# Optimization experiments

Measured on AMD Instinct MI355X. Metric: run time of the kernel, lower is better.

## Reference

```python
import jax, jax.numpy as jnp
import numpy as np

B, H, W, ENC = 64, 14, 14, 2048
A, E, D, V, T = 512, 512, 512, 10000, 21


def setup_inputs() -> dict:
    key = jax.random.key(0)
    ks = jax.random.split(key, 24)
    f = lambda k, shape, s: (jax.random.normal(k, shape, jnp.float32) * s)
    inp = {
        'encoder_out': f(ks[0], (B, H, W, ENC), 1.0),
        'encoded_captions': jax.random.randint(ks[1], (B, T), 0, V),
        'caption_lengths': jax.random.randint(ks[2], (B,), 0, T + 1),
        'emb': jax.random.uniform(ks[3], (V, E), jnp.float32, -0.1, 0.1),
        'enc_att_W': f(ks[4], (ENC, A), 0.02), 'enc_att_b': jnp.zeros((A,), jnp.float32),
        'dec_att_W': f(ks[5], (D, A), 0.04), 'dec_att_b': jnp.zeros((A,), jnp.float32),
        'full_att_W': f(ks[6], (A, 1), 0.04), 'full_att_b': jnp.zeros((1,), jnp.float32),
        'init_h_W': f(ks[7], (ENC, D), 0.02), 'init_h_b': jnp.zeros((D,), jnp.float32),
        'init_c_W': f(ks[8], (ENC, D), 0.02), 'init_c_b': jnp.zeros((D,), jnp.float32),
        'f_beta_W': f(ks[9], (D, ENC), 0.04), 'f_beta_b': jnp.zeros((ENC,), jnp.float32),
        'W_ih': f(ks[10], (4 * D, E + ENC), 0.02), 'b_ih': jnp.zeros((4 * D,), jnp.float32),
        'W_hh': f(ks[11], (4 * D, D), 0.04), 'b_hh': jnp.zeros((4 * D,), jnp.float32),
        'fc_W': jax.random.uniform(ks[12], (D, V), jnp.float32, -0.1, 0.1),
        'fc_b': jnp.zeros((V,), jnp.float32),
    }
    return inp


def reference(encoder_out, encoded_captions, caption_lengths, emb,
              enc_att_W, enc_att_b, dec_att_W, dec_att_b, full_att_W, full_att_b,
              init_h_W, init_h_b, init_c_W, init_c_b, f_beta_W, f_beta_b,
              W_ih, b_ih, W_hh, b_hh, fc_W, fc_b):
    b = encoder_out.shape[0]
    enc = encoder_out.reshape(b, -1, encoder_out.shape[-1])  # (B, P, ENC)
    cl = jnp.clip(caption_lengths.reshape(-1), 1, None)
    sort_ind = jnp.argsort(-cl)  # descending by length
    cl = cl[sort_ind]
    enc = enc[sort_ind]
    caps = encoded_captions[sort_ind]
    dec_len = cl - 1  # (B,)

    embs = emb[caps]  # (B, T, E)
    mean_enc = enc.mean(axis=1)
    h0 = jnp.tanh(mean_enc @ init_h_W + init_h_b)
    c0 = jnp.tanh(mean_enc @ init_c_W + init_c_b)

    att1 = enc @ enc_att_W + enc_att_b  # (B, P, A), loop-invariant
    Tdec = caps.shape[1] - 1
    embs_t = jnp.swapaxes(embs[:, :Tdec], 0, 1)  # (Tdec, B, E)

    def step(carry, xs):
        h, c = carry
        t, x_emb = xs
        active = (t < dec_len)[:, None]  # (B,1)
        att2 = h @ dec_att_W + dec_att_b  # (B, A)
        e = jnp.squeeze(jax.nn.relu(att1 + att2[:, None, :]) @ full_att_W, -1) + full_att_b[0]  # (B,P)
        alpha = jax.nn.softmax(e + 1e-8, axis=1)
        awe = jnp.einsum('bpe,bp->be', enc, alpha)  # (B, ENC)
        gate = jax.nn.sigmoid(h @ f_beta_W + f_beta_b)
        awe = gate * awe
        x = jnp.concatenate([x_emb, awe], axis=1)  # (B, E+ENC)
        gates = x @ W_ih.T + b_ih + h @ W_hh.T + b_hh  # (B, 4D)
        i, f, g, o = jnp.split(gates, 4, axis=1)
        c_new = jax.nn.sigmoid(f) * c + jax.nn.sigmoid(i) * jnp.tanh(g)
        h_new = jax.nn.sigmoid(o) * jnp.tanh(c_new)
        preds = h_new @ fc_W + fc_b
        h = jnp.where(active, h_new, h)
        c = jnp.where(active, c_new, c)
        preds = jnp.where(active, preds, 0.0)
        alpha = jnp.where(active, alpha, 0.0)
        return (h, c), (preds, alpha)

    (_, _), (preds, alphas) = jax.lax.scan(step, (h0, c0), (jnp.arange(Tdec), embs_t))
    predictions = jnp.swapaxes(preds, 0, 1)  # (B, Tdec, V)
    alphas = jnp.swapaxes(alphas, 0, 1)      # (B, Tdec, P)
    return predictions, caps, dec_len, alphas, sort_ind
```

## Files before the change

### kernel.cpp

```cpp
#include <hip/hip_runtime.h>
#include <cstddef>


namespace {

typedef _Float16 f16;
typedef f16 f16x8 __attribute__((ext_vector_type(8)));
typedef f16 f16x4 __attribute__((ext_vector_type(4)));
typedef f16 f16x2 __attribute__((ext_vector_type(2)));
typedef float f32x4 __attribute__((ext_vector_type(4)));

constexpr int NB = 64, NP = 196, NE = 2048, NA = 512, ND = 512, NV = 10000;
constexpr int NT_CAP = 21, NTD = 20;
constexpr int KC = 3072;
constexpr int LDT = 40;
constexpr int LDK = 72;

constexpr size_t OFF_ATT1   = 0;
constexpr size_t OFF_DAW    = 12845056;
constexpr size_t OFF_FBW    = 13369344;
constexpr size_t OFF_EAW    = 15466496;
constexpr size_t OFF_IHW    = 17563648;
constexpr size_t OFF_ICW    = 19660800;
constexpr size_t OFF_FCW    = 15466496;
constexpr size_t OFF_WCAT   = 25755648;
constexpr size_t OFF_MEAN16 = 38338560;
constexpr size_t OFF_H16    = 38600704;
constexpr size_t OFF_HNEW16 = 38666240;
constexpr size_t OFF_C      = 38731776;
constexpr size_t OFF_ATT2   = 38862848;
constexpr size_t OFF_GATE   = 38993920;
constexpr size_t OFF_ALPHA  = 39518208;
constexpr size_t OFF_XCAT   = 39569408;
constexpr size_t OFF_INT    = 39962624;
constexpr size_t OFF_BCAT   = 39970816;
constexpr size_t OFF_ENC16  = 39979008;
constexpr size_t FULL_BYTES = 91359232;
constexpr size_t OFF_HSEQ   = FULL_BYTES;
constexpr size_t FULL2_BYTES = FULL_BYTES + (size_t)NTD * NB * ND * 2;

__device__ __forceinline__ float sigmoidf_(float x) { return 1.0f / (1.0f + expf(-x)); }

__device__ __forceinline__ void stage16(const f16* __restrict__ src, int lda, int k0,
                                        f16* __restrict__ lds, int tid) {
  const int row = tid >> 2, seg = tid & 3;
  *(f16x8*)&lds[row * LDT + seg * 8] =
      *(const f16x8*)&src[(size_t)row * lda + k0 + seg * 8];
}

__device__ __forceinline__ void cvt8(const float* __restrict__ p, f16* __restrict__ dst) {
  const float4 a = *(const float4*)p;
  const float4 b = *(const float4*)(p + 4);
  f16x8 v;
  v[0] = (f16)a.x; v[1] = (f16)a.y; v[2] = (f16)a.z; v[3] = (f16)a.w;
  v[4] = (f16)b.x; v[5] = (f16)b.y; v[6] = (f16)b.z; v[7] = (f16)b.w;
  *(f16x8*)dst = v;
}

__device__ __forceinline__ void wave_gemm64(const f16* __restrict__ A,
                                            const f16* __restrict__ Brow, int K,
                                            int kbeg, int kend,
                                            int col, int quad, f32x4* acc) {
  for (int k0 = kbeg; k0 < kend; k0 += 32) {
    const int kk = k0 + quad * 8;
    const f16x8 b = *(const f16x8*)&Brow[(size_t)col * K + kk];
#pragma unroll
    for (int mt = 0; mt < 4; ++mt) {
      const f16x8 a = *(const f16x8*)&A[(size_t)(mt * 16 + col) * K + kk];
      acc[mt] = __builtin_amdgcn_mfma_f32_16x16x32_f16(a, b, acc[mt], 0, 0, 0);
    }
  }
}

__global__ void k_sort(const int* __restrict__ cap_len, const int* __restrict__ caps,
                       int* __restrict__ perm, int* __restrict__ declen,
                       int* __restrict__ caps_sorted,
                       float* __restrict__ out_caps, float* __restrict__ out_declen,
                       float* __restrict__ out_sortind) {
  __shared__ int cl[NB];
  __shared__ int pr[NB];
  const int i = threadIdx.x;
  int c = cap_len[i];
  if (c < 1) c = 1;
  cl[i] = c;
  __syncthreads();
  int rank = 0;
  for (int j = 0; j < NB; ++j) {
    const int cj = cl[j];
    if (cj > c || (cj == c && j < i)) rank++;
  }
  pr[rank] = i;
  __syncthreads();
  const int src = pr[i];
  perm[i] = src;
  const int dl = cl[src] - 1;
  declen[i] = dl;
  out_declen[i] = (float)dl;
  out_sortind[i] = (float)src;
  for (int j = 0; j < NT_CAP; ++j) {
    const int v = caps[src * NT_CAP + j];
    caps_sorted[i * NT_CAP + j] = v;
    out_caps[i * NT_CAP + j] = (float)v;
  }
}

__global__ __launch_bounds__(256) void k_tconv(const float* __restrict__ src,
                                               f16* __restrict__ dst, int K, int Nsrc) {
  __shared__ float tile[32][33];
  const int n0 = blockIdx.x * 32, k0 = blockIdx.y * 32;
  const int tid = threadIdx.x;
  const int a = tid & 31, q = tid >> 5;
#pragma unroll
  for (int r = 0; r < 4; ++r) {
    const int kl = q * 4 + r;
    tile[a][kl] = (n0 + a < Nsrc) ? src[(size_t)(k0 + kl) * Nsrc + n0 + a] : 0.0f;
  }
  __syncthreads();
#pragma unroll
  for (int r = 0; r < 4; ++r) {
    const int nl = q * 4 + r;
    dst[(size_t)(n0 + nl) * K + k0 + a] = (f16)tile[nl][a];
  }
}

__global__ __launch_bounds__(256) void k_cvt_wcat2(const float* __restrict__ Wih,
                                                   const float* __restrict__ Whh,
                                                   const float* __restrict__ bih,
                                                   const float* __restrict__ bhh,
                                                   f16* __restrict__ Wcat2,
                                                   float* __restrict__ bcat) {
  const int r = blockIdx.x;
  const int d = r >> 2, g = r & 3;
  const int n = g * 512 + d;
  for (int k = threadIdx.x; k < KC; k += 256) {
    const float v = (k < 2560) ? Wih[(size_t)n * 2560 + k] : Whh[(size_t)n * 512 + (k - 2560)];
    Wcat2[(size_t)r * KC + k] = (f16)v;
  }
  if (threadIdx.x == 0) bcat[r] = bih[n] + bhh[n];
}

__global__ __launch_bounds__(256) void k_mean(const float* __restrict__ enc,
                                              const int* __restrict__ perm,
                                              f16* __restrict__ mean16) {
  const int b = blockIdx.y;
  const int c0 = blockIdx.x * 512 + threadIdx.x * 2;
  const float* base = enc + (size_t)perm[b] * NP * NE + c0;
  float a0 = 0.0f, a1 = 0.0f;
  for (int p = 0; p < NP; ++p) {
    const float2 v = *(const float2*)&base[(size_t)p * NE];
    a0 += v.x; a1 += v.y;
  }
  mean16[(size_t)b * NE + c0] = (f16)(a0 * (1.0f / (float)NP));
  mean16[(size_t)b * NE + c0 + 1] = (f16)(a1 * (1.0f / (float)NP));
}

__global__ __launch_bounds__(256) void k_mean16(const f16* __restrict__ enc16,
                                                f16* __restrict__ mean16) {
  const int b = blockIdx.y;
  const int c0 = blockIdx.x * 512 + threadIdx.x * 2;
  const f16* base = enc16 + (size_t)b * NP * NE + c0;
  float a0 = 0.0f, a1 = 0.0f;
  for (int p = 0; p < NP; ++p) {
    const f16x2 v = *(const f16x2*)&base[(size_t)p * NE];
    a0 += (float)v[0]; a1 += (float)v[1];
  }
  mean16[(size_t)b * NE + c0] = (f16)(a0 * (1.0f / (float)NP));
  mean16[(size_t)b * NE + c0 + 1] = (f16)(a1 * (1.0f / (float)NP));
}

__global__ __launch_bounds__(256) void k_enc_cvt(const float* __restrict__ enc,
                                                 const int* __restrict__ perm,
                                                 f16* __restrict__ enc16) {
  const int p = blockIdx.x, b = blockIdx.y;
  const float* src = enc + ((size_t)perm[b] * NP + p) * NE;
  f16* dst = enc16 + ((size_t)b * NP + p) * NE;
  const int i0 = threadIdx.x * 8;
  cvt8(src + i0, dst + i0);
}

__global__ __launch_bounds__(256) void k_init_mfma(const f16* __restrict__ mean16,
                                                   const f16* __restrict__ ihWt,
                                                   const f16* __restrict__ icWt,
                                                   const float* __restrict__ ihb,
                                                   const float* __restrict__ icb,
                                                   f16* __restrict__ h16,
                                                   float* __restrict__ cst) {
  const int which = blockIdx.y;
  const f16* Wt = which ? icWt : ihWt;
  const float* bias = which ? icb : ihb;
  const int tid = threadIdx.x, lane = tid & 63, wv = tid >> 6;
  const int col = lane & 15, quad = lane >> 4;
  const int nt = blockIdx.x * 4 + wv;
  f32x4 acc[4] = {};
  wave_gemm64(mean16, Wt + (size_t)nt * 16 * NE, NE, 0, NE, col, quad, acc);
  const int n = nt * 16 + col;
#pragma unroll
  for (int mt = 0; mt < 4; ++mt) {
#pragma unroll
    for (int rr = 0; rr < 4; ++rr) {
      const int m = mt * 16 + quad * 4 + rr;
      const float v = tanhf(acc[mt][rr] + bias[n]);
      if (which == 0) h16[(size_t)m * ND + n] = (f16)v;
      else            cst[(size_t)m * ND + n] = v;
    }
  }
}

template <bool E16>
__global__ __launch_bounds__(256) void k_att1_mfma(const float* __restrict__ encf,
                                                   const f16* __restrict__ enc16,
                                                   const int* __restrict__ perm,
                                                   const f16* __restrict__ eaWt,
                                                   const float* __restrict__ eab,
                                                   f16* __restrict__ att1) {
  __shared__ __align__(16) f16 lA[64 * LDT];
  __shared__ __align__(16) f16 lB[128 * LDT];
  __shared__ int rowoff[64];
  const int r0 = blockIdx.y * 64;
  const int n0 = blockIdx.x * 128;
  const int tid = threadIdx.x, lane = tid & 63, wv = tid >> 6;
  const int col = lane & 15, quad = lane >> 4;
  if (!E16) {
    if (tid < 64) {
      const int r = r0 + tid;
      const int b = r / NP, p = r - b * NP;
      rowoff[tid] = (perm[b] * NP + p) * NE;
    }
    __syncthreads();
  }
  f32x4 acc[8] = {};
  for (int k0 = 0; k0 < NE; k0 += 32) {
    if (E16) {
      stage16(enc16 + (size_t)r0 * NE, NE, k0, lA, tid);
    } else {
      const int row = tid >> 2, seg = tid & 3;
      cvt8(encf + (size_t)rowoff[row] + k0 + seg * 8, &lA[row * LDT + seg * 8]);
    }
    {
      const int row0 = tid >> 2, seg = tid & 3;
#pragma unroll
      for (int u = 0; u < 2; ++u) {
        const int row = row0 + 64 * u;
        *(f16x8*)&lB[row * LDT + seg * 8] =
            *(const f16x8*)&eaWt[(size_t)(n0 + row) * NE + k0 + seg * 8];
      }
    }
    __syncthreads();
    const f16x8 a = *(const f16x8*)&lA[(wv * 16 + col) * LDT + quad * 8];
#pragma unroll
    for (int ns = 0; ns < 8; ++ns) {
      const f16x8 b = *(const f16x8*)&lB[(ns * 16 + col) * LDT + quad * 8];
      acc[ns] = __builtin_amdgcn_mfma_f32_16x16x32_f16(a, b, acc[ns], 0, 0, 0);
    }
    __syncthreads();
  }
#pragma unroll
  for (int ns = 0; ns < 8; ++ns) {
    const int n = n0 + ns * 16 + col;
#pragma unroll
    for (int rr = 0; rr < 4; ++rr) {
      const int r = r0 + wv * 16 + quad * 4 + rr;
      att1[(size_t)r * NA + n] = (f16)(acc[ns][rr] + eab[n]);
    }
  }
}

__global__ __launch_bounds__(256) void k_att1_v2(const f16* __restrict__ enc16,
                                                 const f16* __restrict__ eaWt,
                                                 const float* __restrict__ eab,
                                                 f16* __restrict__ att1) {
  __shared__ __align__(16) f16 lA[64 * LDK];
  __shared__ __align__(16) f16 lB[128 * LDK];
  const int r0 = blockIdx.y * 64, n0 = blockIdx.x * 128;
  const int tid = threadIdx.x, lane = tid & 63, wv = tid >> 6;
  const int col = lane & 15, quad = lane >> 4;
  const int wr = wv >> 1, wc = wv & 1;
  const int arow = tid >> 2, aseg = (tid & 3) * 16;
  const int brow = tid >> 1, bseg = (tid & 1) * 32;
  const f16* gA = enc16 + (size_t)(r0 + arow) * NE + aseg;
  const f16* gB = eaWt + (size_t)(n0 + brow) * NE + bseg;
  f16* wA = &lA[arow * LDK + aseg];
  f16* wB = &lB[brow * LDK + bseg];
  f32x4 acc[2][4] = {};
  for (int k0 = 0; k0 < NE; k0 += 64) {
    *(f16x8*)(wA)      = *(const f16x8*)(gA + k0);
    *(f16x8*)(wA + 8)  = *(const f16x8*)(gA + k0 + 8);
    *(f16x8*)(wB)      = *(const f16x8*)(gB + k0);
    *(f16x8*)(wB + 8)  = *(const f16x8*)(gB + k0 + 8);
    *(f16x8*)(wB + 16) = *(const f16x8*)(gB + k0 + 16);
    *(f16x8*)(wB + 24) = *(const f16x8*)(gB + k0 + 24);
    __syncthreads();
#pragma unroll
    for (int kh = 0; kh < 2; ++kh) {
      f16x8 a[2], b[4];
#pragma unroll
      for (int i = 0; i < 2; ++i)
        a[i] = *(const f16x8*)&lA[(wr * 32 + i * 16 + col) * LDK + kh * 32 + quad * 8];
#pragma unroll
      for (int j = 0; j < 4; ++j)
        b[j] = *(const f16x8*)&lB[(wc * 64 + j * 16 + col) * LDK + kh * 32 + quad * 8];
#pragma unroll
      for (int i = 0; i < 2; ++i)
#pragma unroll
        for (int j = 0; j < 4; ++j)
          acc[i][j] = __builtin_amdgcn_mfma_f32_16x16x32_f16(a[i], b[j], acc[i][j], 0, 0, 0);
    }
    __syncthreads();
  }
#pragma unroll
  for (int j = 0; j < 4; ++j) {
    const int n = n0 + wc * 64 + j * 16 + col;
    const float bv = eab[n];
#pragma unroll
    for (int i = 0; i < 2; ++i)
#pragma unroll
      for (int rr = 0; rr < 4; ++rr) {
        const int r = r0 + wr * 32 + i * 16 + quad * 4 + rr;
        att1[(size_t)r * NA + n] = (f16)(acc[i][j][rr] + bv);
      }
  }
}

__global__ __launch_bounds__(256) void k_hgemm_v2(const f16* __restrict__ h16,
                                                  const f16* __restrict__ daWt,
                                                  const float* __restrict__ dab,
                                                  const f16* __restrict__ fbWt,
                                                  const float* __restrict__ fbb,
                                                  float* __restrict__ att2,
                                                  float* __restrict__ gate) {
  __shared__ float R[2 * 64 * 16];
  const int tid = threadIdx.x, lane = tid & 63, wv = tid >> 6;
  const int col = lane & 15, quad = lane >> 4;
  const int sub = wv >> 1, kh = wv & 1;
  const int nt = blockIdx.x * 2 + sub;
  const bool is_att = nt < 32;
  const f16* Brow = is_att ? (daWt + (size_t)nt * 16 * ND)
                           : (fbWt + (size_t)(nt - 32) * 16 * ND);
  f32x4 acc[4] = {};
  wave_gemm64(h16, Brow, ND, kh * 256, kh * 256 + 256, col, quad, acc);
  if (kh) {
#pragma unroll
    for (int mt = 0; mt < 4; ++mt)
#pragma unroll
      for (int rr = 0; rr < 4; ++rr)
        R[(sub * 64 + lane) * 16 + mt * 4 + rr] = acc[mt][rr];
  }
  __syncthreads();
  if (kh) return;
#pragma unroll
  for (int mt = 0; mt < 4; ++mt)
#pragma unroll
    for (int rr = 0; rr < 4; ++rr)
      acc[mt][rr] += R[(sub * 64 + lane) * 16 + mt * 4 + rr];
  if (is_att) {
    const int n = nt * 16 + col;
#pragma unroll
    for (int mt = 0; mt < 4; ++mt)
#pragma unroll
      for (int rr = 0; rr < 4; ++rr) {
        const int m = mt * 16 + quad * 4 + rr;
        att2[(size_t)m * NA + n] = acc[mt][rr] + dab[n];
      }
  } else {
    const int n = (nt - 32) * 16 + col;
#pragma unroll
    for (int mt = 0; mt < 4; ++mt)
#pragma unroll
      for (int rr = 0; rr < 4; ++rr) {
        const int m = mt * 16 + quad * 4 + rr;
        gate[(size_t)m * NE + n] = sigmoidf_(acc[mt][rr] + fbb[n]);
      }
  }
}

template <bool E16>
__global__ __launch_bounds__(512) void k_attn_awe(const f16* __restrict__ att1,
                                                  const float* __restrict__ att2,
                                                  const float* __restrict__ fullW,
                                                  const int* __restrict__ declen, int t,
                                                  const float* __restrict__ encf,
                                                  const f16* __restrict__ enc16,
                                                  const int* __restrict__ perm,
                                                  const float* __restrict__ gate,
                                                  const float* __restrict__ emb,
                                                  const int* __restrict__ caps_s,
                                                  const f16* __restrict__ h16,
                                                  f16* __restrict__ xcat,
                                                  float* __restrict__ out_alphas) {
  const int b = blockIdx.x;
  const int tid = threadIdx.x, wv = tid >> 6, lane = tid & 63;
  __shared__ float e[200];
  __shared__ float al[200];
  __shared__ float red2[2];
  {
    float a2r[8], fwr[8];
    const float4* A2 = (const float4*)(att2 + (size_t)b * NA + lane * 8);
    const float4* FW = (const float4*)(fullW + lane * 8);
    const float4 q0 = A2[0], q1 = A2[1], w0 = FW[0], w1 = FW[1];
    a2r[0] = q0.x; a2r[1] = q0.y; a2r[2] = q0.z; a2r[3] = q0.w;
    a2r[4] = q1.x; a2r[5] = q1.y; a2r[6] = q1.z; a2r[7] = q1.w;
    fwr[0] = w0.x; fwr[1] = w0.y; fwr[2] = w0.z; fwr[3] = w0.w;
    fwr[4] = w1.x; fwr[5] = w1.y; fwr[6] = w1.z; fwr[7] = w1.w;
    for (int p = wv; p < NP; p += 8) {
      const f16x8 row = *(const f16x8*)(att1 + ((size_t)b * NP + p) * NA + lane * 8);
      float acc = 0.0f;
#pragma unroll
      for (int j = 0; j < 8; ++j) acc += fmaxf((float)row[j] + a2r[j], 0.0f) * fwr[j];
#pragma unroll
      for (int off = 32; off > 0; off >>= 1) acc += __shfl_down(acc, off, 64);
      if (lane == 0) e[p] = acc;
    }
  }
  __syncthreads();
  if (wv == 0) {
    const float v0 = e[lane];
    const float v1 = e[lane + 64];
    const float v2 = e[lane + 128];
    const float v3 = (lane < 4) ? e[192 + lane] : -INFINITY;
    float mx = fmaxf(fmaxf(v0, v1), fmaxf(v2, v3));
#pragma unroll
    for (int off = 32; off > 0; off >>= 1) mx = fmaxf(mx, __shfl_xor(mx, off, 64));
    float s = expf(v0 - mx) + expf(v1 - mx) + expf(v2 - mx) +
              ((lane < 4) ? expf(v3 - mx) : 0.0f);
#pragma unroll
    for (int off = 32; off > 0; off >>= 1) s += __shfl_xor(s, off, 64);
    if (lane == 0) { red2[0] = mx; red2[1] = 1.0f / s; }
  }
  __syncthreads();
  {
    const float mx = red2[0], inv = red2[1];
    if (tid < NP) {
      const float a = expf(e[tid] - mx) * inv;
      al[tid] = a;
      const bool act = t < declen[b];
      out_alphas[((size_t)b * NTD + t) * NP + tid] = act ? a : 0.0f;
    }
  }
  __syncthreads();
  {
    const int c = tid * 4;
    float a0 = 0.0f, a1 = 0.0f, a2 = 0.0f, a3 = 0.0f;
    if (E16) {
      const f16* base = enc16 + (size_t)b * NP * NE + c;
      for (int p = 0; p < NP; ++p) {
        const f16x4 v = *(const f16x4*)&base[(size_t)p * NE];
        const float ap = al[p];
        a0 += ap * (float)v[0]; a1 += ap * (float)v[1];
        a2 += ap * (float)v[2]; a3 += ap * (float)v[3];
      }
    } else {
      const float* base = encf + (size_t)perm[b] * NP * NE + c;
      for (int p = 0; p < NP; ++p) {
        const float4 v = *(const float4*)&base[(size_t)p * NE];
        const float ap = al[p];
        a0 += ap * v.x; a1 += ap * v.y; a2 += ap * v.z; a3 += ap * v.w;
      }
    }
    const float4 g = *(const float4*)&gate[(size_t)b * NE + c];
    f16x4 o;
    o[0] = (f16)(a0 * g.x); o[1] = (f16)(a1 * g.y);
    o[2] = (f16)(a2 * g.z); o[3] = (f16)(a3 * g.w);
    *(f16x4*)&xcat[(size_t)b * KC + 512 + c] = o;
  }
  if (tid < 256) {
    const int cap = caps_s[b * NT_CAP + t];
    const int i0 = tid * 2;
    const float2 v = *(const float2*)(emb + (size_t)cap * 512 + i0);
    f16x2 ev; ev[0] = (f16)v.x; ev[1] = (f16)v.y;
    *(f16x2*)&xcat[(size_t)b * KC + i0] = ev;
    *(f16x2*)&xcat[(size_t)b * KC + 2560 + i0] = *(const f16x2*)&h16[(size_t)b * ND + i0];
  }
}

__global__ __launch_bounds__(512) void k_xlstm_v2(const f16* __restrict__ xcat,
                                                  const f16* __restrict__ Wcat2,
                                                  const float* __restrict__ bcat,
                                                  const int* __restrict__ declen, int t,
                                                  float* __restrict__ cst,
                                                  f16* __restrict__ h16,
                                                  f16* __restrict__ hnew16,
                                                  f16* __restrict__ hseq) {
  __shared__ float R[8 * 64 * 16];
  const int nt = blockIdx.x;
  const int tid = threadIdx.x, lane = tid & 63, wv = tid >> 6;
  const int col = lane & 15, quad = lane >> 4;
  f32x4 acc[4] = {};
  wave_gemm64(xcat, Wcat2 + (size_t)nt * 16 * KC, KC, wv * 384, wv * 384 + 384,
              col, quad, acc);
#pragma unroll
  for (int mt = 0; mt < 4; ++mt)
#pragma unroll
    for (int rr = 0; rr < 4; ++rr)
      R[(wv * 64 + lane) * 16 + mt * 4 + rr] = acc[mt][rr];
  __syncthreads();
  {
    const int j0 = tid * 2;
#pragma unroll
    for (int j = 0; j < 2; ++j) {
      const int e2 = j0 + j;
      float s = R[e2];
#pragma unroll
      for (int w = 1; w < 8; ++w) s += R[w * 1024 + e2];
      R[e2] = s;
    }
  }
  __syncthreads();
  if (tid < 256) {
    const int m = tid >> 2, dl = tid & 3;
    const int mt = m >> 4, qd = (m >> 2) & 3, rr = m & 3;
    float g4[4];
#pragma unroll
    for (int g = 0; g < 4; ++g) {
      const int cv = dl * 4 + g;
      g4[g] = R[(qd * 16 + cv) * 16 + mt * 4 + rr] + bcat[nt * 16 + cv];
    }
    const int d = nt * 4 + dl;
    const float iv = sigmoidf_(g4[0]);
    const float fv = sigmoidf_(g4[1]);
    const float gv = tanhf(g4[2]);
    const float ov = sigmoidf_(g4[3]);
    const float cold = cst[(size_t)m * ND + d];
    const float cn = fv * cold + iv * gv;
    const float hn = ov * tanhf(cn);
    hnew16[(size_t)m * ND + d] = (f16)hn;
    if (hseq) hseq[((size_t)t * NB + m) * ND + d] = (f16)hn;
    if (t < declen[m]) {
      cst[(size_t)m * ND + d] = cn;
      h16[(size_t)m * ND + d] = (f16)hn;
    }
  }
}

__global__ __launch_bounds__(256) void k_fc_mfma(const f16* __restrict__ hnew16,
                                                 const f16* __restrict__ fcWt,
                                                 const float* __restrict__ fcb,
                                                 const int* __restrict__ declen, int t,
                                                 float* __restrict__ out_pred) {
  const int tid = threadIdx.x, lane = tid & 63, wv = tid >> 6;
  const int col = lane & 15, quad = lane >> 4;
  const int nt = blockIdx.x * 4 + wv;
  f32x4 acc[4] = {};
  wave_gemm64(hnew16, fcWt + (size_t)nt * 16 * ND, ND, 0, ND, col, quad, acc);
  const int n = nt * 16 + col;
  if (n < NV) {
    const float bv = fcb[n];
#pragma unroll
    for (int mt = 0; mt < 4; ++mt)
#pragma unroll
      for (int rr = 0; rr < 4; ++rr) {
        const int m = mt * 16 + quad * 4 + rr;
        const bool act = t < declen[m];
        out_pred[((size_t)m * NTD + t) * NV + n] = act ? (acc[mt][rr] + bv) : 0.0f;
      }
  }
}

__global__ __launch_bounds__(256) void k_fc_v2(const f16* __restrict__ hseq,
                                               const f16* __restrict__ fcWt,
                                               const float* __restrict__ fcb,
                                               const int* __restrict__ declen,
                                               float* __restrict__ out_pred) {
  __shared__ __align__(16) f16 lA[256 * LDK];
  __shared__ __align__(16) f16 lB[64 * LDK];
  const int n0 = blockIdx.x * 64, m0 = blockIdx.y * 256;
  const int tid = threadIdx.x, lane = tid & 63, wv = tid >> 6;
  const int col = lane & 15, quad = lane >> 4;
  const f16* gA = hseq + (size_t)(m0 + tid) * ND;
  const f16* gB = fcWt + (size_t)(n0 + (tid >> 2)) * ND + (tid & 3) * 16;
  f16* wA = &lA[tid * LDK];
  f16* wB = &lB[(tid >> 2) * LDK + (tid & 3) * 16];
  f32x4 acc[4][4] = {};
  for (int k0 = 0; k0 < ND; k0 += 64) {
#pragma unroll
    for (int u = 0; u < 8; ++u)
      *(f16x8*)(wA + u * 8) = *(const f16x8*)(gA + k0 + u * 8);
    *(f16x8*)(wB)     = *(const f16x8*)(gB + k0);
    *(f16x8*)(wB + 8) = *(const f16x8*)(gB + k0 + 8);
    __syncthreads();
#pragma unroll
    for (int kh = 0; kh < 2; ++kh) {
      f16x8 a[4], b[4];
#pragma unroll
      for (int i = 0; i < 4; ++i)
        a[i] = *(const f16x8*)&lA[(wv * 64 + i * 16 + col) * LDK + kh * 32 + quad * 8];
#pragma unroll
      for (int j = 0; j < 4; ++j)
        b[j] = *(const f16x8*)&lB[(j * 16 + col) * LDK + kh * 32 + quad * 8];
#pragma unroll
      for (int i = 0; i < 4; ++i)
#pragma unroll
        for (int j = 0; j < 4; ++j)
          acc[i][j] = __builtin_amdgcn_mfma_f32_16x16x32_f16(a[i], b[j], acc[i][j], 0, 0, 0);
    }
    __syncthreads();
  }
#pragma unroll
  for (int j = 0; j < 4; ++j) {
    const int n = n0 + j * 16 + col;
    if (n >= NV) continue;
    const float bv = fcb[n];
#pragma unroll
    for (int i = 0; i < 4; ++i)
#pragma unroll
      for (int rr = 0; rr < 4; ++rr) {
        const int r = m0 + wv * 64 + i * 16 + quad * 4 + rr;
        const int tt = r >> 6, m = r & 63;
        const bool act = tt < declen[m];
        out_pred[((size_t)m * NTD + tt) * NV + n] = act ? (acc[i][j][rr] + bv) : 0.0f;
      }
  }
}

}

extern "C" void kernel_launch(void* const* d_in, const int* in_sizes, int n_in,
                              void* d_out, int out_size, void* d_ws, size_t ws_size,
                              hipStream_t stream) {
  const float* enc        = (const float*)d_in[0];
  const int*   caps       = (const int*)d_in[1];
  const int*   caplen     = (const int*)d_in[2];
  const float* emb        = (const float*)d_in[3];
  const float* enc_att_W  = (const float*)d_in[4];
  const float* enc_att_b  = (const float*)d_in[5];
  const float* dec_att_W  = (const float*)d_in[6];
  const float* dec_att_b  = (const float*)d_in[7];
  const float* full_att_W = (const float*)d_in[8];
  const float* init_h_W   = (const float*)d_in[10];
  const float* init_h_b   = (const float*)d_in[11];
  const float* init_c_W   = (const float*)d_in[12];
  const float* init_c_b   = (const float*)d_in[13];
  const float* f_beta_W   = (const float*)d_in[14];
  const float* f_beta_b   = (const float*)d_in[15];
  const float* W_ih       = (const float*)d_in[16];
  const float* b_ih       = (const float*)d_in[17];
  const float* W_hh       = (const float*)d_in[18];
  const float* b_hh       = (const float*)d_in[19];
  const float* fc_W       = (const float*)d_in[20];
  const float* fc_b       = (const float*)d_in[21];

  char* ws = (char*)d_ws;
  f16*   att1   = (f16*)(ws + OFF_ATT1);
  f16*   daWt   = (f16*)(ws + OFF_DAW);
  f16*   fbWt   = (f16*)(ws + OFF_FBW);
  f16*   eaWt   = (f16*)(ws + OFF_EAW);
  f16*   ihWt   = (f16*)(ws + OFF_IHW);
  f16*   icWt   = (f16*)(ws + OFF_ICW);
  f16*   fcWt   = (f16*)(ws + OFF_FCW);
  f16*   Wcat2  = (f16*)(ws + OFF_WCAT);
  f16*   mean16 = (f16*)(ws + OFF_MEAN16);
  f16*   h16    = (f16*)(ws + OFF_H16);
  f16*   hnew16 = (f16*)(ws + OFF_HNEW16);
  float* cst    = (float*)(ws + OFF_C);
  float* att2   = (float*)(ws + OFF_ATT2);
  float* gate   = (float*)(ws + OFF_GATE);
  f16*   xcat   = (f16*)(ws + OFF_XCAT);
  int*   wsi    = (int*)(ws + OFF_INT);
  int*   perm   = wsi;
  int*   declen = wsi + 64;
  int*   caps_s = wsi + 128;
  float* bcat   = (float*)(ws + OFF_BCAT);
  f16*   enc16  = (f16*)(ws + OFF_ENC16);

  const bool full  = ws_size >= FULL_BYTES;
  const bool batch = ws_size >= FULL2_BYTES;
  f16* hseq = batch ? (f16*)(ws + OFF_HSEQ) : (f16*)nullptr;

  float* out         = (float*)d_out;
  float* out_pred    = out;
  float* out_caps    = out_pred + (size_t)NB * NTD * NV;
  float* out_declen  = out_caps + (size_t)NB * NT_CAP;
  float* out_alphas  = out_declen + NB;
  float* out_sortind = out_alphas + (size_t)NB * NTD * NP;

  k_sort<<<1, 64, 0, stream>>>(caplen, caps, perm, declen, caps_s,
                               out_caps, out_declen, out_sortind);
  k_tconv<<<dim3(16, 64), 256, 0, stream>>>(enc_att_W, eaWt, 2048, 512);
  k_tconv<<<dim3(16, 16), 256, 0, stream>>>(dec_att_W, daWt, 512, 512);
  k_tconv<<<dim3(64, 16), 256, 0, stream>>>(f_beta_W, fbWt, 512, 2048);
  k_tconv<<<dim3(16, 64), 256, 0, stream>>>(init_h_W, ihWt, 2048, 512);
  k_tconv<<<dim3(16, 64), 256, 0, stream>>>(init_c_W, icWt, 2048, 512);
  if (full) {
    k_enc_cvt<<<dim3(196, 64), 256, 0, stream>>>(enc, perm, enc16);
    k_mean16<<<dim3(4, 64), 256, 0, stream>>>(enc16, mean16);
  } else {
    k_mean<<<dim3(4, 64), 256, 0, stream>>>(enc, perm, mean16);
  }
  k_init_mfma<<<dim3(16, 2), 256, 0, stream>>>(mean16, ihWt, icWt, init_h_b, init_c_b,
                                               h16, cst);
  if (full)
    k_att1_v2<<<dim3(4, 196), 256, 0, stream>>>(enc16, eaWt, enc_att_b, att1);
  else
    k_att1_mfma<false><<<dim3(4, 196), 256, 0, stream>>>(enc, enc16, perm, eaWt,
                                                         enc_att_b, att1);
  k_tconv<<<dim3(314, 16), 256, 0, stream>>>(fc_W, fcWt, 512, NV);
  k_cvt_wcat2<<<2048, 256, 0, stream>>>(W_ih, W_hh, b_ih, b_hh, Wcat2, bcat);

  for (int t = 0; t < NTD; ++t) {
    k_hgemm_v2<<<80, 256, 0, stream>>>(h16, daWt, dec_att_b, fbWt, f_beta_b,
                                       att2, gate);
    if (full)
      k_attn_awe<true><<<NB, 512, 0, stream>>>(att1, att2, full_att_W, declen, t,
                                               enc, enc16, perm, gate, emb, caps_s,
                                               h16, xcat, out_alphas);
    else
      k_attn_awe<false><<<NB, 512, 0, stream>>>(att1, att2, full_att_W, declen, t,
                                                enc, enc16, perm, gate, emb, caps_s,
                                                h16, xcat, out_alphas);
    k_xlstm_v2<<<128, 512, 0, stream>>>(xcat, Wcat2, bcat, declen, t,
                                        cst, h16, hnew16, hseq);
    if (!batch)
      k_fc_mfma<<<157, 256, 0, stream>>>(hnew16, fcWt, fc_b, declen, t, out_pred);
  }
  if (batch)
    k_fc_v2<<<dim3(157, 5), 256, 0, stream>>>(hseq, fcWt, fc_b, declen, out_pred);
}
```

Measured before the change: 1.543 ms.

## Hoist embedding input GEMM out of decode loop and split attention step kernels

Precomputes emb·W_ih for all timesteps in a single batched GEMM before the recurrence. The per-step h·W_hh product is merged into the same h-GEMM kernel as the attention and gate projections, with split-K and an LDS reduction. The attention step is split into a logits/softmax kernel and a wider-grid AWE kernel, and the LSTM GEMM then only covers the AWE part of K with a finer grid. The intent is to shrink per-step sequential GEMM work and raise parallelism on the critical path. In exchange it needs extra workspace, launches one more kernel per step, and takes the new path only if the workspace is large enough.

Result: faster. 1.304 ms (-15.5%).

```diff
diff --git a/kernel.cpp b/kernel.cpp
--- a/kernel.cpp
+++ b/kernel.cpp
@@ -38,6 +38,10 @@
 constexpr size_t FULL_BYTES = 91359232;
 constexpr size_t OFF_HSEQ   = FULL_BYTES;
 constexpr size_t FULL2_BYTES = FULL_BYTES + (size_t)NTD * NB * ND * 2;
+constexpr size_t OFF_HWHH   = FULL2_BYTES;
+constexpr size_t OFF_EMBW   = OFF_HWHH + 524288;
+constexpr size_t OFF_EMBS   = OFF_EMBW + 10485760;
+constexpr size_t FULL3_BYTES = OFF_EMBS + 1310720;
 
 __device__ __forceinline__ float sigmoidf_(float x) { return 1.0f / (1.0f + expf(-x)); }
 
@@ -67,6 +71,22 @@
 #pragma unroll
     for (int mt = 0; mt < 4; ++mt) {
       const f16x8 a = *(const f16x8*)&A[(size_t)(mt * 16 + col) * K + kk];
+      acc[mt] = __builtin_amdgcn_mfma_f32_16x16x32_f16(a, b, acc[mt], 0, 0, 0);
+    }
+  }
+}
+
+template <int MT>
+__device__ __forceinline__ void wave_gemm_s(const f16* __restrict__ A, int lda,
+                                            const f16* __restrict__ Brow, int ldb,
+                                            int kbeg, int kend,
+                                            int col, int quad, f32x4* acc) {
+  for (int k0 = kbeg; k0 < kend; k0 += 32) {
+    const int kk = k0 + quad * 8;
+    const f16x8 b = *(const f16x8*)&Brow[(size_t)col * ldb + kk];
+#pragma unroll
+    for (int mt = 0; mt < MT; ++mt) {
+      const f16x8 a = *(const f16x8*)&A[(size_t)(mt * 16 + col) * lda + kk];
       acc[mt] = __builtin_amdgcn_mfma_f32_16x16x32_f16(a, b, acc[mt], 0, 0, 0);
     }
   }
@@ -176,6 +196,67 @@
   f16* dst = enc16 + ((size_t)b * NP + p) * NE;
   const int i0 = threadIdx.x * 8;
   cvt8(src + i0, dst + i0);
+}
+
+__global__ __launch_bounds__(256) void k_embs(const float* __restrict__ emb,
+                                              const int* __restrict__ caps_s,
+                                              f16* __restrict__ embs16) {
+  const int t = blockIdx.x, b = blockIdx.y;
+  const int cap = caps_s[b * NT_CAP + t];
+  const int i0 = threadIdx.x * 2;
+  const float2 v = *(const float2*)(emb + (size_t)cap * 512 + i0);
+  f16x2 ev; ev[0] = (f16)v.x; ev[1] = (f16)v.y;
+  *(f16x2*)&embs16[((size_t)t * NB + b) * 512 + i0] = ev;
+}
+
+__global__ __launch_bounds__(256) void k_embw(const f16* __restrict__ embs16,
+                                              const f16* __restrict__ Wcat2,
+                                              float* __restrict__ embw) {
+  __shared__ __align__(16) f16 lA[256 * LDK];
+  __shared__ __align__(16) f16 lB[64 * LDK];
+  const int n0 = blockIdx.x * 64, m0 = blockIdx.y * 256;
+  const int tid = threadIdx.x, lane = tid & 63, wv = tid >> 6;
+  const int col = lane & 15, quad = lane >> 4;
+  const f16* gA = embs16 + (size_t)(m0 + tid) * 512;
+  const f16* gB = Wcat2 + (size_t)(n0 + (tid >> 2)) * KC + (tid & 3) * 16;
+  f16* wA = &lA[tid * LDK];
+  f16* wB = &lB[(tid >> 2) * LDK + (tid & 3) * 16];
+  f32x4 acc[4][4] = {};
+  for (int k0 = 0; k0 < 512; k0 += 64) {
+#pragma unroll
+    for (int u = 0; u < 8; ++u)
+      *(f16x8*)(wA + u * 8) = *(const f16x8*)(gA + k0 + u * 8);
+    *(f16x8*)(wB)     = *(const f16x8*)(gB + k0);
+    *(f16x8*)(wB + 8) = *(const f16x8*)(gB + k0 + 8);
+    __syncthreads();
+#pragma unroll
+    for (int kh = 0; kh < 2; ++kh) {
+      f16x8 a[4], b[4];
+#pragma unroll
+      for (int i = 0; i < 4; ++i)
+        a[i] = *(const f16x8*)&lA[(wv * 64 + i * 16 + col) * LDK + kh * 32 + quad * 8];
+#pragma unroll
+      for (int j = 0; j < 4; ++j)
+        b[j] = *(const f16x8*)&lB[(j * 16 + col) * LDK + kh * 32 + quad * 8];
+#pragma unroll
+      for (int i = 0; i < 4; ++i)
+#pragma unroll
+        for (int j = 0; j < 4; ++j)
+          acc[i][j] = __builtin_amdgcn_mfma_f32_16x16x32_f16(a[i], b[j], acc[i][j], 0, 0, 0);
+    }
+    __syncthreads();
+  }
+#pragma unroll
+  for (int j = 0; j < 4; ++j) {
+    const int n = n0 + j * 16 + col;
+#pragma unroll
+    for (int i = 0; i < 4; ++i)
+#pragma unroll
+      for (int rr = 0; rr < 4; ++rr) {
+        const int r = m0 + wv * 64 + i * 16 + quad * 4 + rr;
+        embw[(size_t)r * NE + n] = acc[i][j][rr];
+      }
+  }
 }
 
 __global__ __launch_bounds__(256) void k_init_mfma(const f16* __restrict__ mean16,
@@ -271,7 +352,7 @@
                                                  f16* __restrict__ att1) {
   __shared__ __align__(16) f16 lA[64 * LDK];
   __shared__ __align__(16) f16 lB[128 * LDK];
-  const int r0 = blockIdx.y * 64, n0 = blockIdx.x * 128;
+  const int r0 = blockIdx.x * 64, n0 = blockIdx.y * 128;
   const int tid = threadIdx.x, lane = tid & 63, wv = tid >> 6;
   const int col = lane & 15, quad = lane >> 4;
   const int wr = wv >> 1, wc = wv & 1;
@@ -371,6 +452,131 @@
         gate[(size_t)m * NE + n] = sigmoidf_(acc[mt][rr] + fbb[n]);
       }
   }
+}
+
+__global__ __launch_bounds__(256) void k_hall(const f16* __restrict__ h16,
+                                              const f16* __restrict__ daWt,
+                                              const float* __restrict__ dab,
+                                              const f16* __restrict__ fbWt,
+                                              const float* __restrict__ fbb,
+                                              const f16* __restrict__ Wcat2,
+                                              float* __restrict__ att2,
+                                              float* __restrict__ gate,
+                                              float* __restrict__ hwhh) {
+  __shared__ float R[4 * 1024];
+  const int nt = blockIdx.x;
+  const int tid = threadIdx.x, lane = tid & 63, wv = tid >> 6;
+  const int col = lane & 15, quad = lane >> 4;
+  const f16* Brow; int ldb;
+  if (nt < 32)       { Brow = daWt + (size_t)nt * 16 * ND; ldb = ND; }
+  else if (nt < 160) { Brow = fbWt + (size_t)(nt - 32) * 16 * ND; ldb = ND; }
+  else               { Brow = Wcat2 + (size_t)(nt - 160) * 16 * KC + 2560; ldb = KC; }
+  f32x4 acc[4] = {};
+  wave_gemm_s<4>(h16, ND, Brow, ldb, wv * 128, wv * 128 + 128, col, quad, acc);
+#pragma unroll
+  for (int mt = 0; mt < 4; ++mt)
+#pragma unroll
+    for (int rr = 0; rr < 4; ++rr)
+      R[wv * 1024 + (mt * 4 + rr) * 64 + lane] = acc[mt][rr];
+  __syncthreads();
+#pragma unroll
+  for (int j = 0; j < 4; ++j) {
+    const int slot = tid * 4 + j;
+    const float s = R[slot] + R[1024 + slot] + R[2048 + slot] + R[3072 + slot];
+    const int c2 = slot >> 6;
+    const int lane_s = slot & 63;
+    const int mt = c2 >> 2, rr = c2 & 3;
+    const int m = mt * 16 + (lane_s >> 4) * 4 + rr;
+    const int nl = lane_s & 15;
+    if (nt < 32) {
+      const int n = nt * 16 + nl;
+      att2[(size_t)m * NA + n] = s + dab[n];
+    } else if (nt < 160) {
+      const int n = (nt - 32) * 16 + nl;
+      gate[(size_t)m * NE + n] = sigmoidf_(s + fbb[n]);
+    } else {
+      const int r = (nt - 160) * 16 + nl;
+      hwhh[(size_t)m * NE + r] = s;
+    }
+  }
+}
+
+__global__ __launch_bounds__(512) void k_logits(const f16* __restrict__ att1,
+                                                const float* __restrict__ att2,
+                                                const float* __restrict__ fullW,
+                                                const int* __restrict__ declen, int t,
+                                                float* __restrict__ alpha_ws,
+                                                float* __restrict__ out_alphas) {
+  const int b = blockIdx.x;
+  const int tid = threadIdx.x, wv = tid >> 6, lane = tid & 63;
+  __shared__ float e[200];
+  __shared__ float red2[2];
+  {
+    float a2r[8], fwr[8];
+    const float4* A2 = (const float4*)(att2 + (size_t)b * NA + lane * 8);
+    const float4* FW = (const float4*)(fullW + lane * 8);
+    const float4 q0 = A2[0], q1 = A2[1], w0 = FW[0], w1 = FW[1];
+    a2r[0] = q0.x; a2r[1] = q0.y; a2r[2] = q0.z; a2r[3] = q0.w;
+    a2r[4] = q1.x; a2r[5] = q1.y; a2r[6] = q1.z; a2r[7] = q1.w;
+    fwr[0] = w0.x; fwr[1] = w0.y; fwr[2] = w0.z; fwr[3] = w0.w;
+    fwr[4] = w1.x; fwr[5] = w1.y; fwr[6] = w1.z; fwr[7] = w1.w;
+    for (int p = wv; p < NP; p += 8) {
+      const f16x8 row = *(const f16x8*)(att1 + ((size_t)b * NP + p) * NA + lane * 8);
+      float acc = 0.0f;
+#pragma unroll
+      for (int j = 0; j < 8; ++j) acc += fmaxf((float)row[j] + a2r[j], 0.0f) * fwr[j];
+#pragma unroll
+      for (int off = 32; off > 0; off >>= 1) acc += __shfl_down(acc, off, 64);
+      if (lane == 0) e[p] = acc;
+    }
+  }
+  __syncthreads();
+  if (wv == 0) {
+    const float v0 = e[lane];
+    const float v1 = e[lane + 64];
+    const float v2 = e[lane + 128];
+    const float v3 = (lane < 4) ? e[192 + lane] : -INFINITY;
+    float mx = fmaxf(fmaxf(v0, v1), fmaxf(v2, v3));
+#pragma unroll
+    for (int off = 32; off > 0; off >>= 1) mx = fmaxf(mx, __shfl_xor(mx, off, 64));
+    float s = expf(v0 - mx) + expf(v1 - mx) + expf(v2 - mx) +
+              ((lane < 4) ? expf(v3 - mx) : 0.0f);
+#pragma unroll
+    for (int off = 32; off > 0; off >>= 1) s += __shfl_xor(s, off, 64);
+    if (lane == 0) { red2[0] = mx; red2[1] = 1.0f / s; }
+  }
+  __syncthreads();
+  if (tid < NP) {
+    const float a = expf(e[tid] - red2[0]) * red2[1];
+    alpha_ws[(size_t)b * NP + tid] = a;
+    const bool act = t < declen[b];
+    out_alphas[((size_t)b * NTD + t) * NP + tid] = act ? a : 0.0f;
+  }
+}
+
+__global__ __launch_bounds__(256) void k_awe(const f16* __restrict__ enc16,
+                                             const float* __restrict__ alpha_ws,
+                                             const float* __restrict__ gate,
+                                             f16* __restrict__ xcat) {
+  const int b = blockIdx.x >> 2, q = blockIdx.x & 3;
+  const int tid = threadIdx.x;
+  __shared__ float al[NP];
+  if (tid < NP) al[tid] = alpha_ws[(size_t)b * NP + tid];
+  __syncthreads();
+  const int c = q * 512 + tid * 2;
+  const f16* base = enc16 + (size_t)b * NP * NE + c;
+  float a0 = 0.0f, a1 = 0.0f, b0 = 0.0f, b1 = 0.0f;
+  for (int p = 0; p < NP; p += 2) {
+    const f16x2 v0 = *(const f16x2*)&base[(size_t)p * NE];
+    const f16x2 v1 = *(const f16x2*)&base[(size_t)(p + 1) * NE];
+    const float ap0 = al[p], ap1 = al[p + 1];
+    a0 += ap0 * (float)v0[0]; a1 += ap0 * (float)v0[1];
+    b0 += ap1 * (float)v1[0]; b1 += ap1 * (float)v1[1];
+  }
+  a0 += b0; a1 += b1;
+  const float2 g = *(const float2*)&gate[(size_t)b * NE + c];
+  f16x2 o; o[0] = (f16)(a0 * g.x); o[1] = (f16)(a1 * g.y);
+  *(f16x2*)&xcat[(size_t)b * KC + 512 + c] = o;
 }
 
 template <bool E16>
@@ -531,6 +737,67 @@
   }
 }
 
+__global__ __launch_bounds__(512) void k_xlstm_v3(const f16* __restrict__ xcat,
+                                                  const f16* __restrict__ Wcat2,
+                                                  const float* __restrict__ bcat,
+                                                  const float* __restrict__ hwhh,
+                                                  const float* __restrict__ embw,
+                                                  const int* __restrict__ declen, int t,
+                                                  float* __restrict__ cst,
+                                                  f16* __restrict__ h16,
+                                                  f16* __restrict__ hnew16,
+                                                  f16* __restrict__ hseq) {
+  __shared__ float R[8 * 512];
+  const int nt = blockIdx.x >> 1, mh = blockIdx.x & 1;
+  const int tid = threadIdx.x, lane = tid & 63, wv = tid >> 6;
+  const int col = lane & 15, quad = lane >> 4;
+  f32x4 acc[2] = {};
+  wave_gemm_s<2>(xcat + (size_t)mh * 32 * KC, KC,
+                 Wcat2 + (size_t)nt * 16 * KC, KC,
+                 512 + wv * 256, 512 + wv * 256 + 256, col, quad, acc);
+#pragma unroll
+  for (int mt = 0; mt < 2; ++mt)
+#pragma unroll
+    for (int rr = 0; rr < 4; ++rr)
+      R[wv * 512 + (mt * 4 + rr) * 64 + lane] = acc[mt][rr];
+  __syncthreads();
+  {
+    float s = R[tid];
+#pragma unroll
+    for (int w = 1; w < 8; ++w) s += R[w * 512 + tid];
+    R[tid] = s;
+  }
+  __syncthreads();
+  if (tid < 128) {
+    const int ml = tid >> 2, dl = tid & 3;
+    const int m = mh * 32 + ml;
+    const int d = nt * 4 + dl;
+    const int mt = ml >> 4, qd = (ml >> 2) & 3, rr = ml & 3;
+    float g4[4];
+#pragma unroll
+    for (int g = 0; g < 4; ++g) {
+      const int cv = dl * 4 + g;
+      const int r = nt * 16 + cv;
+      const float s = R[(mt * 4 + rr) * 64 + qd * 16 + cv];
+      g4[g] = s + bcat[r] + hwhh[(size_t)m * NE + r] +
+              embw[((size_t)t * NB + m) * NE + r];
+    }
+    const float iv = sigmoidf_(g4[0]);
+    const float fv = sigmoidf_(g4[1]);
+    const float gv = tanhf(g4[2]);
+    const float ov = sigmoidf_(g4[3]);
+    const float cold = cst[(size_t)m * ND + d];
+    const float cn = fv * cold + iv * gv;
+    const float hn = ov * tanhf(cn);
+    hnew16[(size_t)m * ND + d] = (f16)hn;
+    hseq[((size_t)t * NB + m) * ND + d] = (f16)hn;
+    if (t < declen[m]) {
+      cst[(size_t)m * ND + d] = cn;
+      h16[(size_t)m * ND + d] = (f16)hn;
+    }
+  }
+}
+
 __global__ __launch_bounds__(256) void k_fc_mfma(const f16* __restrict__ hnew16,
                                                  const f16* __restrict__ fcWt,
                                                  const float* __restrict__ fcb,
@@ -653,6 +920,7 @@
   float* cst    = (float*)(ws + OFF_C);
   float* att2   = (float*)(ws + OFF_ATT2);
   float* gate   = (float*)(ws + OFF_GATE);
+  float* alpha  = (float*)(ws + OFF_ALPHA);
   f16*   xcat   = (f16*)(ws + OFF_XCAT);
   int*   wsi    = (int*)(ws + OFF_INT);
   int*   perm   = wsi;
@@ -660,9 +928,13 @@
   int*   caps_s = wsi + 128;
   float* bcat   = (float*)(ws + OFF_BCAT);
   f16*   enc16  = (f16*)(ws + OFF_ENC16);
+  float* hwhh   = (float*)(ws + OFF_HWHH);
+  float* embw   = (float*)(ws + OFF_EMBW);
+  f16*   embs16 = (f16*)(ws + OFF_EMBS);
 
   const bool full  = ws_size >= FULL_BYTES;
   const bool batch = ws_size >= FULL2_BYTES;
+  const bool full3 = ws_size >= FULL3_BYTES;
   f16* hseq = batch ? (f16*)(ws + OFF_HSEQ) : (f16*)nullptr;
 
   float* out         = (float*)d_out;
@@ -688,29 +960,46 @@
   k_init_mfma<<<dim3(16, 2), 256, 0, stream>>>(mean16, ihWt, icWt, init_h_b, init_c_b,
                                                h16, cst);
   if (full)
-    k_att1_v2<<<dim3(4, 196), 256, 0, stream>>>(enc16, eaWt, enc_att_b, att1);
+    k_att1_v2<<<dim3(196, 4), 256, 0, stream>>>(enc16, eaWt, enc_att_b, att1);
   else
     k_att1_mfma<false><<<dim3(4, 196), 256, 0, stream>>>(enc, enc16, perm, eaWt,
                                                          enc_att_b, att1);
   k_tconv<<<dim3(314, 16), 256, 0, stream>>>(fc_W, fcWt, 512, NV);
   k_cvt_wcat2<<<2048, 256, 0, stream>>>(W_ih, W_hh, b_ih, b_hh, Wcat2, bcat);
-
-  for (int t = 0; t < NTD; ++t) {
-    k_hgemm_v2<<<80, 256, 0, stream>>>(h16, daWt, dec_att_b, fbWt, f_beta_b,
-                                       att2, gate);
-    if (full)
-      k_attn_awe<true><<<NB, 512, 0, stream>>>(att1, att2, full_att_W, declen, t,
-                                               enc, enc16, perm, gate, emb, caps_s,
-                                               h16, xcat, out_alphas);
-    else
-      k_attn_awe<false><<<NB, 512, 0, stream>>>(att1, att2, full_att_W, declen, t,
-                                                enc, enc16, perm, gate, emb, caps_s,
-                                                h16, xcat, out_alphas);
-    k_xlstm_v2<<<128, 512, 0, stream>>>(xcat, Wcat2, bcat, declen, t,
-                                        cst, h16, hnew16, hseq);
-    if (!batch)
-      k_fc_mfma<<<157, 256, 0, stream>>>(hnew16, fcWt, fc_b, declen, t, out_pred);
-  }
-  if (batch)
+  if (full3) {
+    k_embs<<<dim3(NTD, NB), 256, 0, stream>>>(emb, caps_s, embs16);
+    k_embw<<<dim3(32, 5), 256, 0, stream>>>(embs16, Wcat2, embw);
+  }
+
+  if (full3) {
+    for (int t = 0; t < NTD; ++t) {
+      k_hall<<<288, 256, 0, stream>>>(h16, daWt, dec_att_b, fbWt, f_beta_b, Wcat2,
+                                      att2, gate, hwhh);
+      k_logits<<<NB, 512, 0, stream>>>(att1, att2, full_att_W, declen, t,
+                                       alpha, out_alphas);
+      k_awe<<<256, 256, 0, stream>>>(enc16, alpha, gate, xcat);
+      k_xlstm_v3<<<256, 512, 0, stream>>>(xcat, Wcat2, bcat, hwhh, embw, declen, t,
+                                          cst, h16, hnew16, hseq);
+    }
     k_fc_v2<<<dim3(157, 5), 256, 0, stream>>>(hseq, fcWt, fc_b, declen, out_pred);
-}
+  } else {
+    for (int t = 0; t < NTD; ++t) {
+      k_hgemm_v2<<<80, 256, 0, stream>>>(h16, daWt, dec_att_b, fbWt, f_beta_b,
+                                         att2, gate);
+      if (full)
+        k_attn_awe<true><<<NB, 512, 0, stream>>>(att1, att2, full_att_W, declen, t,
+                                                 enc, enc16, perm, gate, emb, caps_s,
+                                                 h16, xcat, out_alphas);
+      else
+        k_attn_awe<false><<<NB, 512, 0, stream>>>(att1, att2, full_att_W, declen, t,
+                                                  enc, enc16, perm, gate, emb, caps_s,
+                                                  h16, xcat, out_alphas);
+      k_xlstm_v2<<<128, 512, 0, stream>>>(xcat, Wcat2, bcat, declen, t,
+                                          cst, h16, hnew16, hseq);
+      if (!batch)
+        k_fc_mfma<<<157, 256, 0, stream>>>(hnew16, fcWt, fc_b, declen, t, out_pred);
+    }
+    if (batch)
+      k_fc_v2<<<dim3(157, 5), 256, 0, stream>>>(hseq, fcWt, fc_b, declen, out_pred);
+  }
+}
```
